# Kernel tuning notes

Hardware: AMD Instinct MI355X
Metric: run time of the kernel (lower is better)

## Reference

```python
import jax, jax.numpy as jnp
import numpy as np
import math

B, L, P, D, H, RBF = 4, 256, 1024, 512, 8, 50
d = D // H  # head_dim = 64
EPS = 1e-5


def setup_inputs() -> dict:
    key = jax.random.key(0)
    ks = jax.random.split(key, 20)
    s = 1.0 / math.sqrt(D)
    inp = {
        "query": jax.random.normal(ks[0], (B, L, D), jnp.float32),
        "key": jax.random.normal(ks[1], (B, P, D), jnp.float32),
        "value": jax.random.normal(ks[2], (B, P, D), jnp.float32),
        "cross_rbf": jax.random.uniform(ks[3], (B, L, P, RBF), jnp.float32),
        "key_mask": jax.random.randint(ks[4], (B, P), 0, 2, jnp.int32),
        "Wq": jax.random.normal(ks[5], (D, D), jnp.float32) * s,
        "bq": jnp.zeros((D,), jnp.float32),
        "Wk": jax.random.normal(ks[6], (D, D), jnp.float32) * s,
        "bk": jnp.zeros((D,), jnp.float32),
        "Wv": jax.random.normal(ks[7], (D, D), jnp.float32) * s,
        "bv": jnp.zeros((D,), jnp.float32),
        "Wr": jax.random.normal(ks[8], (RBF, H), jnp.float32) * (1.0 / math.sqrt(RBF)),
        "br": jnp.zeros((H,), jnp.float32),
        "Wo": jax.random.normal(ks[9], (D, D), jnp.float32) * s,
        "bo": jnp.zeros((D,), jnp.float32),
        "gamma": jnp.ones((D,), jnp.float32),
        "beta": jnp.zeros((D,), jnp.float32),
    }
    return inp


def reference(query, key, value, cross_rbf, key_mask,
              Wq, bq, Wk, bk, Wv, bv, Wr, br, Wo, bo, gamma, beta):
    Q = (query @ Wq + bq).reshape(B, L, H, d)
    K = (key @ Wk + bk).reshape(B, P, H, d)
    V = (value @ Wv + bv).reshape(B, P, H, d)
    # scores [B, L, P, H]
    attn = jnp.einsum('blhd,bphd->blph', Q, K) / math.sqrt(d)
    dist_bias = cross_rbf @ Wr + br  # [B, L, P, H]
    attn = attn + dist_bias
    attn = jnp.where(key_mask[:, None, :, None] == 0, -1e9, attn)
    attn = jax.nn.softmax(attn, axis=2)  # softmax over P
    out = jnp.einsum('blph,bphd->blhd', attn, V).reshape(B, L, D)
    out = out @ Wo + bo
    x = query + out
    mu = jnp.mean(x, axis=-1, keepdims=True)
    var = jnp.mean((x - mu) ** 2, axis=-1, keepdims=True)
    normed = (x - mu) / jnp.sqrt(var + EPS) * gamma + beta
    return normed, attn.mean(axis=-1)
```

## Files before the change

### kernel.cpp

```cpp
#include <hip/hip_runtime.h>
#include <hip/hip_bf16.h>

#define BB 4
#define LL 256
#define PP 1024
#define DD 512
#define HH 8
#define HD 64
#define NRBF 50

__device__ __forceinline__ float bf2f(unsigned short u) {
  return __uint_as_float((unsigned)u << 16);
}

__device__ __forceinline__ float ldf(const void* p, size_t i, bool f32) {
  if (f32) return ((const float*)p)[i];
  return bf2f(((const unsigned short*)p)[i]);
}

__device__ __forceinline__ float4 ld4e(const void* p, size_t i, bool f32) {
  if (f32) return *(const float4*)((const float*)p + i);
  ushort4 u = *(const ushort4*)((const unsigned short*)p + i);
  float4 r;
  r.x = bf2f(u.x); r.y = bf2f(u.y); r.z = bf2f(u.z); r.w = bf2f(u.w);
  return r;
}

__global__ __launch_bounds__(256) void detect_dtype(const float* q, int* flag) {
  __shared__ int cnt;
  if (threadIdx.x == 0) cnt = 0;
  __syncthreads();
  int c = 0;
  for (int i = threadIdx.x; i < 1024; i += 256) {
    unsigned u = __float_as_uint(q[i]);
    unsigned e = (u >> 23) & 0xffu;
    if (e >= 104u && e <= 140u) c++;
  }
  atomicAdd(&cnt, c);
  __syncthreads();
  if (threadIdx.x == 0) *flag = (cnt > 512) ? 1 : 0;
}

__device__ void gemm128(const void* __restrict__ X, const void* __restrict__ W,
                        const void* __restrict__ bias, float* __restrict__ Y,
                        const int bm, const int bn, const int mode,
                        const bool f32, float* lds) {
  const int tid = threadIdx.x;
  const int tx = tid & 15, ty = tid >> 4;
  const int lr = tid >> 1, lc = (tid & 1) * 8;
  const int wk = tid >> 5, wc = (tid & 31) * 4;
  float acc[8][8] = {};
  float4 ra0, ra1, rb0, rb1;

  ra0 = ld4e(X, (size_t)(bm + lr) * 512 + lc, f32);
  ra1 = ld4e(X, (size_t)(bm + lr) * 512 + lc + 4, f32);
  rb0 = ld4e(W, (size_t)wk * 512 + bn + wc, f32);
  rb1 = ld4e(W, (size_t)(wk + 8) * 512 + bn + wc, f32);
  {
    float* Ab = lds;
    float* Bb = lds + 4096;
    Ab[(lc + 0) * 128 + lr] = ra0.x; Ab[(lc + 1) * 128 + lr] = ra0.y;
    Ab[(lc + 2) * 128 + lr] = ra0.z; Ab[(lc + 3) * 128 + lr] = ra0.w;
    Ab[(lc + 4) * 128 + lr] = ra1.x; Ab[(lc + 5) * 128 + lr] = ra1.y;
    Ab[(lc + 6) * 128 + lr] = ra1.z; Ab[(lc + 7) * 128 + lr] = ra1.w;
    *(float4*)&Bb[wk * 128 + wc] = rb0;
    *(float4*)&Bb[(wk + 8) * 128 + wc] = rb1;
  }
  __syncthreads();

  int buf = 0;
  for (int tt = 0; tt < 32; ++tt) {
    if (tt < 31) {
      const int k0 = (tt + 1) * 16;
      ra0 = ld4e(X, (size_t)(bm + lr) * 512 + k0 + lc, f32);
      ra1 = ld4e(X, (size_t)(bm + lr) * 512 + k0 + lc + 4, f32);
      rb0 = ld4e(W, (size_t)(k0 + wk) * 512 + bn + wc, f32);
      rb1 = ld4e(W, (size_t)(k0 + wk + 8) * 512 + bn + wc, f32);
    }
    {
      const float* Ab = lds + buf * 2048;
      const float* Bb = lds + 4096 + buf * 2048;
#pragma unroll
      for (int k = 0; k < 16; ++k) {
        float4 aL = *(const float4*)&Ab[k * 128 + ty * 4];
        float4 aH = *(const float4*)&Ab[k * 128 + 64 + ty * 4];
        float4 bL = *(const float4*)&Bb[k * 128 + tx * 4];
        float4 bH = *(const float4*)&Bb[k * 128 + 64 + tx * 4];
        const float a8[8] = {aL.x, aL.y, aL.z, aL.w, aH.x, aH.y, aH.z, aH.w};
        const float b8[8] = {bL.x, bL.y, bL.z, bL.w, bH.x, bH.y, bH.z, bH.w};
#pragma unroll
        for (int i = 0; i < 8; ++i)
#pragma unroll
          for (int j = 0; j < 8; ++j)
            acc[i][j] = fmaf(a8[i], b8[j], acc[i][j]);
      }
    }
    if (tt < 31) {
      float* Ab = lds + (buf ^ 1) * 2048;
      float* Bb = lds + 4096 + (buf ^ 1) * 2048;
      Ab[(lc + 0) * 128 + lr] = ra0.x; Ab[(lc + 1) * 128 + lr] = ra0.y;
      Ab[(lc + 2) * 128 + lr] = ra0.z; Ab[(lc + 3) * 128 + lr] = ra0.w;
      Ab[(lc + 4) * 128 + lr] = ra1.x; Ab[(lc + 5) * 128 + lr] = ra1.y;
      Ab[(lc + 6) * 128 + lr] = ra1.z; Ab[(lc + 7) * 128 + lr] = ra1.w;
      *(float4*)&Bb[wk * 128 + wc] = rb0;
      *(float4*)&Bb[(wk + 8) * 128 + wc] = rb1;
    }
    __syncthreads();
    buf ^= 1;
  }

  if (mode == 0) {
#pragma unroll
    for (int rh = 0; rh < 2; ++rh)
#pragma unroll
      for (int i = 0; i < 4; ++i) {
        const int r = bm + rh * 64 + ty * 4 + i;
#pragma unroll
        for (int ch = 0; ch < 2; ++ch) {
          const int c = bn + ch * 64 + tx * 4;
          float4 o;
          o.x = acc[rh * 4 + i][ch * 4 + 0] + ldf(bias, c + 0, f32);
          o.y = acc[rh * 4 + i][ch * 4 + 1] + ldf(bias, c + 1, f32);
          o.z = acc[rh * 4 + i][ch * 4 + 2] + ldf(bias, c + 2, f32);
          o.w = acc[rh * 4 + i][ch * 4 + 3] + ldf(bias, c + 3, f32);
          *(float4*)&Y[(size_t)r * 512 + c] = o;
        }
      }
  } else {
    const int bq = bm >> 10;
    const int pb = bm & 1023;
#pragma unroll
    for (int ch = 0; ch < 2; ++ch)
#pragma unroll
      for (int j = 0; j < 4; ++j) {
        const int c = bn + ch * 64 + tx * 4 + j;
        const float bb = ldf(bias, c, f32);
#pragma unroll
        for (int rh = 0; rh < 2; ++rh) {
          float4 pv;
          pv.x = acc[rh * 4 + 0][ch * 4 + j] + bb;
          pv.y = acc[rh * 4 + 1][ch * 4 + j] + bb;
          pv.z = acc[rh * 4 + 2][ch * 4 + j] + bb;
          pv.w = acc[rh * 4 + 3][ch * 4 + j] + bb;
          const int p0 = pb + rh * 64 + ty * 4;
          *(float4*)&Y[(((size_t)bq * 8 + (c >> 6)) * 64 + (c & 63)) * 1024 +
                       p0] = pv;
        }
      }
  }
}

__global__ __launch_bounds__(256) void fused_qkvr(
    const void* __restrict__ query, const void* __restrict__ key,
    const void* __restrict__ value, const void* __restrict__ Wq,
    const void* __restrict__ bq_, const void* __restrict__ Wk,
    const void* __restrict__ bk_, const void* __restrict__ Wv,
    const void* __restrict__ bv_, const void* __restrict__ rbf,
    const void* __restrict__ Wr, const void* __restrict__ br_,
    float* __restrict__ Qw, float* __restrict__ Ktw, float* __restrict__ Vw,
    float* __restrict__ biasW, const int* __restrict__ flag) {
  __shared__ float lds[8192];
  const bool f32 = (*flag != 0);
  const int blk = blockIdx.x;

  if (blk < 288) {
    const void *X, *W, *bias;
    float* Y;
    int mode, mi, ni;
    if (blk < 32) {
      X = query; W = Wq; bias = bq_; Y = Qw; mode = 0;
      mi = blk >> 2; ni = blk & 3;
    } else if (blk < 160) {
      const int q2 = blk - 32;
      X = key; W = Wk; bias = bk_; Y = Ktw; mode = 1;
      mi = q2 >> 2; ni = q2 & 3;
    } else {
      const int q2 = blk - 160;
      X = value; W = Wv; bias = bv_; Y = Vw; mode = 0;
      mi = q2 >> 2; ni = q2 & 3;
    }
    gemm128(X, W, bias, Y, mi * 128, ni * 128, mode, f32, lds);
    return;
  }

  float* wrS = lds;
  float* brS = lds + 404;
  const int tid = threadIdx.x;
  for (int i = tid; i < NRBF * 8; i += 256) wrS[i] = ldf(Wr, i, f32);
  if (tid < 8) brS[tid] = ldf(br_, tid, f32);
  __syncthreads();
  const size_t row = (size_t)(blk - 288) * 256 + tid;
  float acc[8];
#pragma unroll
  for (int h = 0; h < 8; ++h) acc[h] = brS[h];
  if (f32) {
    const float2* rp = (const float2*)((const float*)rbf + row * NRBF);
#pragma unroll
    for (int j = 0; j < 25; ++j) {
      float2 r2 = rp[j];
      float4 wa = *(const float4*)&wrS[(2 * j) * 8];
      float4 wb = *(const float4*)&wrS[(2 * j) * 8 + 4];
      float4 wc = *(const float4*)&wrS[(2 * j + 1) * 8];
      float4 wd = *(const float4*)&wrS[(2 * j + 1) * 8 + 4];
      acc[0] = fmaf(r2.x, wa.x, acc[0]); acc[1] = fmaf(r2.x, wa.y, acc[1]);
      acc[2] = fmaf(r2.x, wa.z, acc[2]); acc[3] = fmaf(r2.x, wa.w, acc[3]);
      acc[4] = fmaf(r2.x, wb.x, acc[4]); acc[5] = fmaf(r2.x, wb.y, acc[5]);
      acc[6] = fmaf(r2.x, wb.z, acc[6]); acc[7] = fmaf(r2.x, wb.w, acc[7]);
      acc[0] = fmaf(r2.y, wc.x, acc[0]); acc[1] = fmaf(r2.y, wc.y, acc[1]);
      acc[2] = fmaf(r2.y, wc.z, acc[2]); acc[3] = fmaf(r2.y, wc.w, acc[3]);
      acc[4] = fmaf(r2.y, wd.x, acc[4]); acc[5] = fmaf(r2.y, wd.y, acc[5]);
      acc[6] = fmaf(r2.y, wd.z, acc[6]); acc[7] = fmaf(r2.y, wd.w, acc[7]);
    }
  } else {
    const unsigned short* rb = (const unsigned short*)rbf + row * NRBF;
#pragma unroll
    for (int j = 0; j < NRBF; ++j) {
      float r = bf2f(rb[j]);
#pragma unroll
      for (int h = 0; h < 8; ++h) acc[h] = fmaf(r, wrS[j * 8 + h], acc[h]);
    }
  }
  const size_t bl = row >> 10;
  const int p = (int)(row & 1023);
#pragma unroll
  for (int h = 0; h < 8; ++h) biasW[(bl * 8 + h) * 1024 + p] = acc[h];
}

#define SST 1028

__global__ __launch_bounds__(512) void attn_v6(
    const float* __restrict__ Q,
    const float* __restrict__ Kt,
    const float* __restrict__ V,
    const float* __restrict__ biasW,
    const int* __restrict__ mask,
    float* __restrict__ AO,
    void* __restrict__ d_out, const int* __restrict__ flag) {
  const int xcd = blockIdx.x & 7;
  const int idx = blockIdx.x >> 3;
  const int b = xcd >> 1;
  const int lp = ((xcd & 1) << 6) | idx;
  const int bl0 = b * LL + lp * 2;
  const int t = threadIdx.x;
  const bool f32 = (*flag != 0);

  __shared__ float qS[2][512];
  __shared__ float scoresS[2][8 * SST];

  for (int i = t; i < 1024; i += 512)
    qS[i >> 9][i & 511] = Q[(size_t)bl0 * 512 + i];
  __syncthreads();

  {
    const int tq = t & 255;
    const int hh = t >> 8;
    const int4 mk4 = *(const int4*)(mask + b * PP + 4 * tq);
#pragma unroll 1
    for (int hi = 0; hi < 4; ++hi) {
      const int h = hh * 4 + hi;
      const float4* ktp =
          (const float4*)(Kt + ((size_t)b * 8 + h) * 64 * 1024) + tq;
      float4 a0 = {0.f, 0.f, 0.f, 0.f}, a1 = {0.f, 0.f, 0.f, 0.f};
#pragma unroll 2
      for (int dq = 0; dq < 16; ++dq) {
        float4 qa = *(const float4*)&qS[0][h * 64 + dq * 4];
        float4 qb = *(const float4*)&qS[1][h * 64 + dq * 4];
        float4 k0 = ktp[(size_t)(dq * 4 + 0) * 256];
        float4 k1 = ktp[(size_t)(dq * 4 + 1) * 256];
        float4 k2 = ktp[(size_t)(dq * 4 + 2) * 256];
        float4 k3 = ktp[(size_t)(dq * 4 + 3) * 256];
        a0.x = fmaf(qa.x, k0.x, a0.x); a0.y = fmaf(qa.x, k0.y, a0.y);
        a0.z = fmaf(qa.x, k0.z, a0.z); a0.w = fmaf(qa.x, k0.w, a0.w);
        a0.x = fmaf(qa.y, k1.x, a0.x); a0.y = fmaf(qa.y, k1.y, a0.y);
        a0.z = fmaf(qa.y, k1.z, a0.z); a0.w = fmaf(qa.y, k1.w, a0.w);
        a0.x = fmaf(qa.z, k2.x, a0.x); a0.y = fmaf(qa.z, k2.y, a0.y);
        a0.z = fmaf(qa.z, k2.z, a0.z); a0.w = fmaf(qa.z, k2.w, a0.w);
        a0.x = fmaf(qa.w, k3.x, a0.x); a0.y = fmaf(qa.w, k3.y, a0.y);
        a0.z = fmaf(qa.w, k3.z, a0.z); a0.w = fmaf(qa.w, k3.w, a0.w);
        a1.x = fmaf(qb.x, k0.x, a1.x); a1.y = fmaf(qb.x, k0.y, a1.y);
        a1.z = fmaf(qb.x, k0.z, a1.z); a1.w = fmaf(qb.x, k0.w, a1.w);
        a1.x = fmaf(qb.y, k1.x, a1.x); a1.y = fmaf(qb.y, k1.y, a1.y);
        a1.z = fmaf(qb.y, k1.z, a1.z); a1.w = fmaf(qb.y, k1.w, a1.w);
        a1.x = fmaf(qb.z, k2.x, a1.x); a1.y = fmaf(qb.z, k2.y, a1.y);
        a1.z = fmaf(qb.z, k2.z, a1.z); a1.w = fmaf(qb.z, k2.w, a1.w);
        a1.x = fmaf(qb.w, k3.x, a1.x); a1.y = fmaf(qb.w, k3.y, a1.y);
        a1.z = fmaf(qb.w, k3.z, a1.z); a1.w = fmaf(qb.w, k3.w, a1.w);
      }
      float4 b40 =
          *(const float4*)&biasW[((size_t)bl0 * 8 + h) * 1024 + 4 * tq];
      float4 b41 =
          *(const float4*)&biasW[((size_t)(bl0 + 1) * 8 + h) * 1024 + 4 * tq];
      float4 s0, s1;
      s0.x = (mk4.x == 0) ? -1e9f : fmaf(a0.x, 0.125f, b40.x);
      s0.y = (mk4.y == 0) ? -1e9f : fmaf(a0.y, 0.125f, b40.y);
      s0.z = (mk4.z == 0) ? -1e9f : fmaf(a0.z, 0.125f, b40.z);
      s0.w = (mk4.w == 0) ? -1e9f : fmaf(a0.w, 0.125f, b40.w);
      s1.x = (mk4.x == 0) ? -1e9f : fmaf(a1.x, 0.125f, b41.x);
      s1.y = (mk4.y == 0) ? -1e9f : fmaf(a1.y, 0.125f, b41.y);
      s1.z = (mk4.z == 0) ? -1e9f : fmaf(a1.z, 0.125f, b41.z);
      s1.w = (mk4.w == 0) ? -1e9f : fmaf(a1.w, 0.125f, b41.w);
      *(float4*)&scoresS[0][h * SST + 4 * tq] = s0;
      *(float4*)&scoresS[1][h * SST + 4 * tq] = s1;
    }
  }
  __syncthreads();

  {
    const int wave = t >> 6, lane = t & 63;
    for (int pr = wave * 2; pr < wave * 2 + 2; ++pr) {
      float* sc = &scoresS[pr >> 3][(pr & 7) * SST];
      float m = -3.0e38f;
      for (int i = lane; i < PP; i += 64) m = fmaxf(m, sc[i]);
#pragma unroll
      for (int off = 32; off; off >>= 1) m = fmaxf(m, __shfl_xor(m, off, 64));
      float sum = 0.f;
      for (int i = lane; i < PP; i += 64) {
        float e = __expf(sc[i] - m);
        sc[i] = e;
        sum += e;
      }
#pragma unroll
      for (int off = 32; off; off >>= 1) sum += __shfl_xor(sum, off, 64);
      const float inv = 1.0f / sum;
      for (int i = lane; i < PP; i += 64) sc[i] *= inv;
    }
  }
  __syncthreads();

  {
    const int q = t >> 8, pq = t & 255;
    float4 s = {0.f, 0.f, 0.f, 0.f};
#pragma unroll
    for (int h = 0; h < 8; ++h) {
      float4 v = *(const float4*)&scoresS[q][h * SST + 4 * pq];
      s.x += v.x; s.y += v.y; s.z += v.z; s.w += v.w;
    }
    s.x *= 0.125f; s.y *= 0.125f; s.z *= 0.125f; s.w *= 0.125f;
    const size_t base =
        (size_t)BB * LL * DD + (size_t)(bl0 + q) * PP + 4 * pq;
    if (f32) {
      *(float4*)((float*)d_out + base) = s;
    } else {
      __hip_bfloat16* o1 = (__hip_bfloat16*)d_out;
      o1[base + 0] = __float2bfloat16(s.x);
      o1[base + 1] = __float2bfloat16(s.y);
      o1[base + 2] = __float2bfloat16(s.z);
      o1[base + 3] = __float2bfloat16(s.w);
    }
  }

  float4 pa0, pa1;
  {
    const int cq = t & 127;
    const int ph = t >> 7;
    const int h = cq >> 4;
    const float* sc0 = &scoresS[0][h * SST];
    const float* sc1 = &scoresS[1][h * SST];
    const float4* Vb = (const float4*)(V + (size_t)b * PP * 512) + cq;
    float4 A0 = {0.f, 0.f, 0.f, 0.f}, A1 = {0.f, 0.f, 0.f, 0.f};
    const int p0 = ph * 256;
#pragma unroll 2
    for (int p4 = p0; p4 < p0 + 256; p4 += 4) {
      float4 pr0 = *(const float4*)&sc0[p4];
      float4 pr1 = *(const float4*)&sc1[p4];
      float4 v0 = Vb[(size_t)(p4 + 0) * 128];
      float4 v1 = Vb[(size_t)(p4 + 1) * 128];
      float4 v2 = Vb[(size_t)(p4 + 2) * 128];
      float4 v3 = Vb[(size_t)(p4 + 3) * 128];
      A0.x = fmaf(pr0.x, v0.x, A0.x); A0.y = fmaf(pr0.x, v0.y, A0.y);
      A0.z = fmaf(pr0.x, v0.z, A0.z); A0.w = fmaf(pr0.x, v0.w, A0.w);
      A0.x = fmaf(pr0.y, v1.x, A0.x); A0.y = fmaf(pr0.y, v1.y, A0.y);
      A0.z = fmaf(pr0.y, v1.z, A0.z); A0.w = fmaf(pr0.y, v1.w, A0.w);
      A0.x = fmaf(pr0.z, v2.x, A0.x); A0.y = fmaf(pr0.z, v2.y, A0.y);
      A0.z = fmaf(pr0.z, v2.z, A0.z); A0.w = fmaf(pr0.z, v2.w, A0.w);
      A0.x = fmaf(pr0.w, v3.x, A0.x); A0.y = fmaf(pr0.w, v3.y, A0.y);
      A0.z = fmaf(pr0.w, v3.z, A0.z); A0.w = fmaf(pr0.w, v3.w, A0.w);
      A1.x = fmaf(pr1.x, v0.x, A1.x); A1.y = fmaf(pr1.x, v0.y, A1.y);
      A1.z = fmaf(pr1.x, v0.z, A1.z); A1.w = fmaf(pr1.x, v0.w, A1.w);
      A1.x = fmaf(pr1.y, v1.x, A1.x); A1.y = fmaf(pr1.y, v1.y, A1.y);
      A1.z = fmaf(pr1.y, v1.z, A1.z); A1.w = fmaf(pr1.y, v1.w, A1.w);
      A1.x = fmaf(pr1.z, v2.x, A1.x); A1.y = fmaf(pr1.z, v2.y, A1.y);
      A1.z = fmaf(pr1.z, v2.z, A1.z); A1.w = fmaf(pr1.z, v2.w, A1.w);
      A1.x = fmaf(pr1.w, v3.x, A1.x); A1.y = fmaf(pr1.w, v3.y, A1.y);
      A1.z = fmaf(pr1.w, v3.z, A1.z); A1.w = fmaf(pr1.w, v3.w, A1.w);
    }
    pa0 = A0;
    pa1 = A1;
  }
  __syncthreads();
  {
    const int cq = t & 127, ph = t >> 7;
    float* parts = &scoresS[0][0];
    *(float4*)&parts[((0 * 4 + ph) * 128 + cq) * 4] = pa0;
    *(float4*)&parts[((1 * 4 + ph) * 128 + cq) * 4] = pa1;
  }
  __syncthreads();
  if (t < 256) {
    const int q = t >> 7, c = t & 127;
    const float* parts = &scoresS[0][0];
    float4 a = *(const float4*)&parts[((q * 4 + 0) * 128 + c) * 4];
#pragma unroll
    for (int ph = 1; ph < 4; ++ph) {
      float4 x = *(const float4*)&parts[((q * 4 + ph) * 128 + c) * 4];
      a.x += x.x; a.y += x.y; a.z += x.z; a.w += x.w;
    }
    *(float4*)&AO[(size_t)(bl0 + q) * 512 + 4 * c] = a;
  }
}

__global__ __launch_bounds__(256) void proj_out(
    const float* __restrict__ X, const void* __restrict__ W,
    const void* __restrict__ bias, const void* __restrict__ resid,
    float* __restrict__ Y, const int* __restrict__ flag) {
  __shared__ float As[16][64];
  __shared__ float Bs[16][64];
  const bool f32 = (*flag != 0);
  const int bm = blockIdx.x * 64, bn = blockIdx.y * 64;
  const int tid = threadIdx.x;
  const int tx = tid & 15, ty = tid >> 4;
  float acc[4][4] = {};
  for (int k0 = 0; k0 < 512; k0 += 16) {
    {
      int r = tid >> 2, kf = (tid & 3) * 4;
      float4 x4 = *(const float4*)(X + (size_t)(bm + r) * 512 + k0 + kf);
      As[kf + 0][r] = x4.x; As[kf + 1][r] = x4.y;
      As[kf + 2][r] = x4.z; As[kf + 3][r] = x4.w;
    }
    if (f32) {
      int kk = tid >> 4, cf = (tid & 15) * 4;
      *(float4*)&Bs[kk][cf] =
          *(const float4*)((const float*)W + (size_t)(k0 + kk) * 512 + bn + cf);
    } else {
      const unsigned short* Wb = (const unsigned short*)W;
      for (int f = tid; f < 16 * 64; f += 256) {
        int kk = f >> 6, c = f & 63;
        Bs[kk][c] = bf2f(Wb[(size_t)(k0 + kk) * 512 + bn + c]);
      }
    }
    __syncthreads();
#pragma unroll
    for (int k = 0; k < 16; ++k) {
      float4 a4 = *(const float4*)&As[k][ty * 4];
      float4 b4 = *(const float4*)&Bs[k][tx * 4];
      acc[0][0] = fmaf(a4.x, b4.x, acc[0][0]); acc[0][1] = fmaf(a4.x, b4.y, acc[0][1]);
      acc[0][2] = fmaf(a4.x, b4.z, acc[0][2]); acc[0][3] = fmaf(a4.x, b4.w, acc[0][3]);
      acc[1][0] = fmaf(a4.y, b4.x, acc[1][0]); acc[1][1] = fmaf(a4.y, b4.y, acc[1][1]);
      acc[1][2] = fmaf(a4.y, b4.z, acc[1][2]); acc[1][3] = fmaf(a4.y, b4.w, acc[1][3]);
      acc[2][0] = fmaf(a4.z, b4.x, acc[2][0]); acc[2][1] = fmaf(a4.z, b4.y, acc[2][1]);
      acc[2][2] = fmaf(a4.z, b4.z, acc[2][2]); acc[2][3] = fmaf(a4.z, b4.w, acc[2][3]);
      acc[3][0] = fmaf(a4.w, b4.x, acc[3][0]); acc[3][1] = fmaf(a4.w, b4.y, acc[3][1]);
      acc[3][2] = fmaf(a4.w, b4.z, acc[3][2]); acc[3][3] = fmaf(a4.w, b4.w, acc[3][3]);
    }
    __syncthreads();
  }
#pragma unroll
  for (int i = 0; i < 4; ++i) {
    int r = bm + ty * 4 + i;
    float4 o;
#pragma unroll
    for (int j = 0; j < 4; ++j) {
      int c = bn + tx * 4 + j;
      float v = acc[i][j] + ldf(bias, c, f32) +
                ldf(resid, (size_t)r * 512 + c, f32);
      ((float*)&o)[j] = v;
    }
    *(float4*)(Y + (size_t)r * 512 + bn + tx * 4) = o;
  }
}

__global__ __launch_bounds__(256) void ln_kernel(
    const float* __restrict__ Xw, const void* __restrict__ gamma,
    const void* __restrict__ beta, void* __restrict__ d_out,
    const int* __restrict__ flag) {
  const int bl = blockIdx.x;
  const int tid = threadIdx.x;
  const bool f32 = (*flag != 0);
  __shared__ float red[16];
  float v0 = Xw[(size_t)bl * 512 + tid];
  float v1 = Xw[(size_t)bl * 512 + tid + 256];
  float s = v0 + v1, s2 = v0 * v0 + v1 * v1;
#pragma unroll
  for (int off = 32; off; off >>= 1) {
    s += __shfl_xor(s, off, 64);
    s2 += __shfl_xor(s2, off, 64);
  }
  const int wave = tid >> 6, lane = tid & 63;
  if (lane == 0) { red[wave] = s; red[8 + wave] = s2; }
  __syncthreads();
  if (tid == 0) {
    float ts = 0.f, ts2 = 0.f;
    for (int w = 0; w < 4; ++w) { ts += red[w]; ts2 += red[8 + w]; }
    red[0] = ts; red[1] = ts2;
  }
  __syncthreads();
  const float mu = red[0] * (1.0f / 512.0f);
  const float var = red[1] * (1.0f / 512.0f) - mu * mu;
  const float rstd = rsqrtf(var + 1e-5f);
  float o0 = (v0 - mu) * rstd * ldf(gamma, tid, f32) + ldf(beta, tid, f32);
  float o1 = (v1 - mu) * rstd * ldf(gamma, tid + 256, f32) +
             ldf(beta, tid + 256, f32);
  if (f32) {
    float* o = (float*)d_out;
    o[(size_t)bl * 512 + tid] = o0;
    o[(size_t)bl * 512 + tid + 256] = o1;
  } else {
    __hip_bfloat16* o = (__hip_bfloat16*)d_out;
    o[(size_t)bl * 512 + tid] = __float2bfloat16(o0);
    o[(size_t)bl * 512 + tid + 256] = __float2bfloat16(o1);
  }
}

extern "C" void kernel_launch(void* const* d_in, const int* in_sizes, int n_in,
                              void* d_out, int out_size, void* d_ws,
                              size_t ws_size, hipStream_t stream) {
  const void* query = d_in[0];
  const void* key = d_in[1];
  const void* value = d_in[2];
  const void* rbf = d_in[3];
  const int* key_mask = (const int*)d_in[4];
  const void* Wq = d_in[5];
  const void* bq = d_in[6];
  const void* Wk = d_in[7];
  const void* bk = d_in[8];
  const void* Wv = d_in[9];
  const void* bv = d_in[10];
  const void* Wr = d_in[11];
  const void* br = d_in[12];
  const void* Wo = d_in[13];
  const void* bo = d_in[14];
  const void* gamma = d_in[15];
  const void* beta = d_in[16];

  int* flag = (int*)d_ws;
  float* base = (float*)d_ws + 4;
  float* Qw = base;
  float* Ktw = Qw + (size_t)BB * LL * DD;
  float* Vw = Ktw + (size_t)BB * PP * DD;
  float* AO = Vw + (size_t)BB * PP * DD;
  float* Xw = AO + (size_t)BB * LL * DD;
  float* biasW = Xw + (size_t)BB * LL * DD;

  detect_dtype<<<1, 256, 0, stream>>>((const float*)query, flag);
  fused_qkvr<<<dim3(288 + 4096), 256, 0, stream>>>(
      query, key, value, Wq, bq, Wk, bk, Wv, bv, rbf, Wr, br, Qw, Ktw, Vw,
      biasW, flag);
  attn_v6<<<dim3(BB * LL / 2), 512, 0, stream>>>(Qw, Ktw, Vw, biasW, key_mask,
                                                 AO, d_out, flag);
  proj_out<<<dim3(16, 8), 256, 0, stream>>>(AO, Wo, bo, query, Xw, flag);
  ln_kernel<<<dim3(BB * LL), 256, 0, stream>>>(Xw, gamma, beta, d_out, flag);
}
```

Measured before the change: 588.1 us.

## Fuse RBF distance-bias projection into attention kernel, drop biasW round trip

Moves the cross_rbf @ Wr + br projection out of the QKV GEMM launch and into the attention kernel. Each attention block computes the bias for its two query rows directly into the shared-memory scores buffer, and the score pass reads it back from LDS instead of from a global biasW buffer. This removes the write and re-read of the B*L*8*P bias tensor. In exchange, the RBF reads (the dominant memory traffic) now sit on the attention kernel's critical path with only 512 blocks, which may lower the memory parallelism available for that stream.

```diff
diff --git a/kernel.cpp b/kernel.cpp
--- a/kernel.cpp
+++ b/kernel.cpp
@@ -150,89 +150,45 @@
   }
 }
 
-__global__ __launch_bounds__(256) void fused_qkvr(
+__global__ __launch_bounds__(256) void qkv_gemm(
     const void* __restrict__ query, const void* __restrict__ key,
     const void* __restrict__ value, const void* __restrict__ Wq,
     const void* __restrict__ bq_, const void* __restrict__ Wk,
     const void* __restrict__ bk_, const void* __restrict__ Wv,
-    const void* __restrict__ bv_, const void* __restrict__ rbf,
-    const void* __restrict__ Wr, const void* __restrict__ br_,
-    float* __restrict__ Qw, float* __restrict__ Ktw, float* __restrict__ Vw,
-    float* __restrict__ biasW, const int* __restrict__ flag) {
+    const void* __restrict__ bv_, float* __restrict__ Qw,
+    float* __restrict__ Ktw, float* __restrict__ Vw,
+    const int* __restrict__ flag) {
   __shared__ float lds[8192];
   const bool f32 = (*flag != 0);
   const int blk = blockIdx.x;
 
-  if (blk < 288) {
-    const void *X, *W, *bias;
-    float* Y;
-    int mode, mi, ni;
-    if (blk < 32) {
-      X = query; W = Wq; bias = bq_; Y = Qw; mode = 0;
-      mi = blk >> 2; ni = blk & 3;
-    } else if (blk < 160) {
-      const int q2 = blk - 32;
-      X = key; W = Wk; bias = bk_; Y = Ktw; mode = 1;
-      mi = q2 >> 2; ni = q2 & 3;
-    } else {
-      const int q2 = blk - 160;
-      X = value; W = Wv; bias = bv_; Y = Vw; mode = 0;
-      mi = q2 >> 2; ni = q2 & 3;
-    }
-    gemm128(X, W, bias, Y, mi * 128, ni * 128, mode, f32, lds);
-    return;
-  }
-
-  float* wrS = lds;
-  float* brS = lds + 404;
-  const int tid = threadIdx.x;
-  for (int i = tid; i < NRBF * 8; i += 256) wrS[i] = ldf(Wr, i, f32);
-  if (tid < 8) brS[tid] = ldf(br_, tid, f32);
-  __syncthreads();
-  const size_t row = (size_t)(blk - 288) * 256 + tid;
-  float acc[8];
-#pragma unroll
-  for (int h = 0; h < 8; ++h) acc[h] = brS[h];
-  if (f32) {
-    const float2* rp = (const float2*)((const float*)rbf + row * NRBF);
-#pragma unroll
-    for (int j = 0; j < 25; ++j) {
-      float2 r2 = rp[j];
-      float4 wa = *(const float4*)&wrS[(2 * j) * 8];
-      float4 wb = *(const float4*)&wrS[(2 * j) * 8 + 4];
-      float4 wc = *(const float4*)&wrS[(2 * j + 1) * 8];
-      float4 wd = *(const float4*)&wrS[(2 * j + 1) * 8 + 4];
-      acc[0] = fmaf(r2.x, wa.x, acc[0]); acc[1] = fmaf(r2.x, wa.y, acc[1]);
-      acc[2] = fmaf(r2.x, wa.z, acc[2]); acc[3] = fmaf(r2.x, wa.w, acc[3]);
-      acc[4] = fmaf(r2.x, wb.x, acc[4]); acc[5] = fmaf(r2.x, wb.y, acc[5]);
-      acc[6] = fmaf(r2.x, wb.z, acc[6]); acc[7] = fmaf(r2.x, wb.w, acc[7]);
-      acc[0] = fmaf(r2.y, wc.x, acc[0]); acc[1] = fmaf(r2.y, wc.y, acc[1]);
-      acc[2] = fmaf(r2.y, wc.z, acc[2]); acc[3] = fmaf(r2.y, wc.w, acc[3]);
-      acc[4] = fmaf(r2.y, wd.x, acc[4]); acc[5] = fmaf(r2.y, wd.y, acc[5]);
-      acc[6] = fmaf(r2.y, wd.z, acc[6]); acc[7] = fmaf(r2.y, wd.w, acc[7]);
-    }
+  const void *X, *W, *bias;
+  float* Y;
+  int mode, mi, ni;
+  if (blk < 32) {
+    X = query; W = Wq; bias = bq_; Y = Qw; mode = 0;
+    mi = blk >> 2; ni = blk & 3;
+  } else if (blk < 160) {
+    const int q2 = blk - 32;
+    X = key; W = Wk; bias = bk_; Y = Ktw; mode = 1;
+    mi = q2 >> 2; ni = q2 & 3;
   } else {
-    const unsigned short* rb = (const unsigned short*)rbf + row * NRBF;
-#pragma unroll
-    for (int j = 0; j < NRBF; ++j) {
-      float r = bf2f(rb[j]);
-#pragma unroll
-      for (int h = 0; h < 8; ++h) acc[h] = fmaf(r, wrS[j * 8 + h], acc[h]);
-    }
-  }
-  const size_t bl = row >> 10;
-  const int p = (int)(row & 1023);
-#pragma unroll
-  for (int h = 0; h < 8; ++h) biasW[(bl * 8 + h) * 1024 + p] = acc[h];
+    const int q2 = blk - 160;
+    X = value; W = Wv; bias = bv_; Y = Vw; mode = 0;
+    mi = q2 >> 2; ni = q2 & 3;
+  }
+  gemm128(X, W, bias, Y, mi * 128, ni * 128, mode, f32, lds);
 }
 
 #define SST 1028
 
-__global__ __launch_bounds__(512) void attn_v6(
+__global__ __launch_bounds__(512) void attn_v7(
     const float* __restrict__ Q,
     const float* __restrict__ Kt,
     const float* __restrict__ V,
-    const float* __restrict__ biasW,
+    const void* __restrict__ rbf,
+    const void* __restrict__ Wr,
+    const void* __restrict__ br_,
     const int* __restrict__ mask,
     float* __restrict__ AO,
     void* __restrict__ d_out, const int* __restrict__ flag) {
@@ -245,10 +201,66 @@
   const bool f32 = (*flag != 0);
 
   __shared__ float qS[2][512];
+  __shared__ float wrS[NRBF * 8];
+  __shared__ float brS[8];
   __shared__ float scoresS[2][8 * SST];
 
   for (int i = t; i < 1024; i += 512)
     qS[i >> 9][i & 511] = Q[(size_t)bl0 * 512 + i];
+  for (int i = t; i < NRBF * 8; i += 512) wrS[i] = ldf(Wr, i, f32);
+  if (t < 8) brS[t] = ldf(br_, t, f32);
+  __syncthreads();
+
+  {
+    const int q = t >> 8;
+    const int tq = t & 255;
+    float acc[4][8];
+#pragma unroll
+    for (int r = 0; r < 4; ++r)
+#pragma unroll
+      for (int h = 0; h < 8; ++h) acc[r][h] = brS[h];
+    const size_t rbase = ((size_t)(bl0 + q) * 1024 + 4 * tq) * NRBF;
+    if (f32) {
+      const float4* r4 = (const float4*)((const float*)rbf + rbase);
+#pragma unroll
+      for (int i = 0; i < 50; ++i) {
+        const float4 v = r4[i];
+        const float vv[4] = {v.x, v.y, v.z, v.w};
+#pragma unroll
+        for (int c = 0; c < 4; ++c) {
+          const int lin = 4 * i + c;
+          const int rr = lin / 50;
+          const int jj = lin - rr * 50;
+          const float4 wa = *(const float4*)&wrS[jj * 8];
+          const float4 wb = *(const float4*)&wrS[jj * 8 + 4];
+          acc[rr][0] = fmaf(vv[c], wa.x, acc[rr][0]);
+          acc[rr][1] = fmaf(vv[c], wa.y, acc[rr][1]);
+          acc[rr][2] = fmaf(vv[c], wa.z, acc[rr][2]);
+          acc[rr][3] = fmaf(vv[c], wa.w, acc[rr][3]);
+          acc[rr][4] = fmaf(vv[c], wb.x, acc[rr][4]);
+          acc[rr][5] = fmaf(vv[c], wb.y, acc[rr][5]);
+          acc[rr][6] = fmaf(vv[c], wb.z, acc[rr][6]);
+          acc[rr][7] = fmaf(vv[c], wb.w, acc[rr][7]);
+        }
+      }
+    } else {
+      const unsigned short* rb = (const unsigned short*)rbf + rbase;
+#pragma unroll 1
+      for (int e = 0; e < 4; ++e)
+        for (int j = 0; j < 50; ++j) {
+          const float rv = bf2f(rb[e * 50 + j]);
+#pragma unroll
+          for (int h = 0; h < 8; ++h)
+            acc[e][h] = fmaf(rv, wrS[j * 8 + h], acc[e][h]);
+        }
+    }
+#pragma unroll
+    for (int h = 0; h < 8; ++h) {
+      float4 o;
+      o.x = acc[0][h]; o.y = acc[1][h]; o.z = acc[2][h]; o.w = acc[3][h];
+      *(float4*)&scoresS[q][h * SST + 4 * tq] = o;
+    }
+  }
   __syncthreads();
 
   {
@@ -286,10 +298,8 @@
         a1.x = fmaf(qb.w, k3.x, a1.x); a1.y = fmaf(qb.w, k3.y, a1.y);
         a1.z = fmaf(qb.w, k3.z, a1.z); a1.w = fmaf(qb.w, k3.w, a1.w);
       }
-      float4 b40 =
-          *(const float4*)&biasW[((size_t)bl0 * 8 + h) * 1024 + 4 * tq];
-      float4 b41 =
-          *(const float4*)&biasW[((size_t)(bl0 + 1) * 8 + h) * 1024 + 4 * tq];
+      float4 b40 = *(const float4*)&scoresS[0][h * SST + 4 * tq];
+      float4 b41 = *(const float4*)&scoresS[1][h * SST + 4 * tq];
       float4 s0, s1;
       s0.x = (mk4.x == 0) ? -1e9f : fmaf(a0.x, 0.125f, b40.x);
       s0.y = (mk4.y == 0) ? -1e9f : fmaf(a0.y, 0.125f, b40.y);
@@ -538,14 +548,12 @@
   float* Vw = Ktw + (size_t)BB * PP * DD;
   float* AO = Vw + (size_t)BB * PP * DD;
   float* Xw = AO + (size_t)BB * LL * DD;
-  float* biasW = Xw + (size_t)BB * LL * DD;
 
   detect_dtype<<<1, 256, 0, stream>>>((const float*)query, flag);
-  fused_qkvr<<<dim3(288 + 4096), 256, 0, stream>>>(
-      query, key, value, Wq, bq, Wk, bk, Wv, bv, rbf, Wr, br, Qw, Ktw, Vw,
-      biasW, flag);
-  attn_v6<<<dim3(BB * LL / 2), 512, 0, stream>>>(Qw, Ktw, Vw, biasW, key_mask,
-                                                 AO, d_out, flag);
+  qkv_gemm<<<dim3(288), 256, 0, stream>>>(query, key, value, Wq, bq, Wk, bk,
+                                          Wv, bv, Qw, Ktw, Vw, flag);
+  attn_v7<<<dim3(BB * LL / 2), 512, 0, stream>>>(Qw, Ktw, Vw, rbf, Wr, br,
+                                                 key_mask, AO, d_out, flag);
   proj_out<<<dim3(16, 8), 256, 0, stream>>>(AO, Wo, bo, query, Xw, flag);
   ln_kernel<<<dim3(BB * LL), 256, 0, stream>>>(Xw, gamma, beta, d_out, flag);
 }
```

Result: slower. 819.9 us (+39.4%).
